# Optimization experiments

Hardware: AMD Instinct MI355X
Metric: run time of the kernel (lower is better)

Reference implementation:

```python
import jax, jax.numpy as jnp
import numpy as np

N_NODES = 100000
N_EDGES = 1600000
IN_C = 128
HID_C = 128   # 2 * out_channels
OUT_C = 64


def gcn_conv(x, row, col, w, W, b, num_nodes):
    """PyG GCNConv: linear transform, add self-loops (weight 1),
    symmetric degree normalization, scatter-sum aggregation, bias."""
    h = x @ W  # [N, C_out]
    loop = jnp.arange(num_nodes, dtype=row.dtype)
    r = jnp.concatenate([row, loop])
    c = jnp.concatenate([col, loop])
    ew = jnp.concatenate([w, jnp.ones((num_nodes,), dtype=w.dtype)])
    deg = jax.ops.segment_sum(ew, c, num_segments=num_nodes)
    dinv = jnp.where(deg > 0, jax.lax.rsqrt(deg), 0.0)
    norm = dinv[r] * ew * dinv[c]            # [E+N]
    msg = h[r] * norm[:, None]               # [E+N, C_out] gather
    out = jax.ops.segment_sum(msg, c, num_segments=num_nodes)
    return out + b


def setup_inputs() -> dict:
    key = jax.random.key(0)
    k1, k2, k3, k4, k5, k6, k7, k8 = jax.random.split(key, 8)
    x = jax.random.normal(k1, (N_NODES, IN_C), dtype=jnp.float32)
    edge_index = jax.random.randint(k2, (2, N_EDGES), 0, N_NODES, dtype=jnp.int64)
    edge_weight = jax.random.uniform(k3, (N_EDGES,), dtype=jnp.float32)
    s1 = float(np.sqrt(6.0 / (IN_C + HID_C)))
    s2 = float(np.sqrt(6.0 / (HID_C + OUT_C)))
    W1 = jax.random.uniform(k4, (IN_C, HID_C), minval=-s1, maxval=s1, dtype=jnp.float32)
    b1 = jnp.zeros((HID_C,), dtype=jnp.float32)
    W2 = jax.random.uniform(k5, (HID_C, OUT_C), minval=-s2, maxval=s2, dtype=jnp.float32)
    b2 = jnp.zeros((OUT_C,), dtype=jnp.float32)
    return {"x": x, "edge_index": edge_index, "edge_weight": edge_weight,
            "W1": W1, "b1": b1, "W2": W2, "b2": b2}


def reference(x, edge_index, edge_weight, W1, b1, W2, b2):
    row, col = edge_index[0], edge_index[1]
    n = x.shape[0]
    h = jax.nn.relu(gcn_conv(x, row, col, edge_weight, W1, b1, n))
    h = jax.nn.relu(gcn_conv(h, row, col, edge_weight, W2, b2, n))
    return h
```

## Files before the change

### kernel.cpp

```cpp
#include <hip/hip_runtime.h>

#define TPB 256

typedef unsigned int uint32;
typedef unsigned short ushort_t;
typedef __attribute__((ext_vector_type(8))) short bf16x8;
typedef __attribute__((ext_vector_type(4))) float f32x4;

constexpr int NB = 256;
constexpr int B1 = 256;

__device__ __forceinline__ uint32 pack_bf16x2(float a, float b) {
  uint32 ua = __float_as_uint(a), ub = __float_as_uint(b);
  ua += 0x7FFFu + ((ua >> 16) & 1u);
  ub += 0x7FFFu + ((ub >> 16) & 1u);
  return (ua >> 16) | (ub & 0xFFFF0000u);
}
__device__ __forceinline__ ushort_t bf16_of(float a) {
  uint32 u = __float_as_uint(a);
  u += 0x7FFFu + ((u >> 16) & 1u);
  return (ushort_t)(u >> 16);
}
__device__ __forceinline__ float bf16_lo(uint32 u) { return __uint_as_float(u << 16); }
__device__ __forceinline__ float bf16_hi(uint32 u) { return __uint_as_float(u & 0xFFFF0000u); }

__global__ __launch_bounds__(256) void rx_hist(const int* __restrict__ col,
                                               int* __restrict__ blockhist, int e, int chunk) {
  __shared__ int h[NB];
  int tid = threadIdx.x, blk = blockIdx.x;
  h[tid] = 0;
  __syncthreads();
  int s = blk * chunk, t = min(e, s + chunk);
  for (int i = s + tid; i < t; i += 256) atomicAdd(&h[col[i] & 255], 1);
  __syncthreads();
  blockhist[tid * B1 + blk] = h[tid];
}

__global__ __launch_bounds__(256) void k_scan1(int* __restrict__ a, int* __restrict__ bsum, int n) {
  __shared__ int s[256];
  int tid = threadIdx.x;
  int base = blockIdx.x * 1024 + tid * 4;
  int v0 = 0, v1 = 0, v2 = 0, v3 = 0;
  if (base + 0 < n) v0 = a[base + 0];
  if (base + 1 < n) v1 = a[base + 1];
  if (base + 2 < n) v2 = a[base + 2];
  if (base + 3 < n) v3 = a[base + 3];
  int tsum = v0 + v1 + v2 + v3;
  s[tid] = tsum;
  __syncthreads();
  for (int off = 1; off < 256; off <<= 1) {
    int t = (tid >= off) ? s[tid - off] : 0;
    __syncthreads();
    s[tid] += t;
    __syncthreads();
  }
  if (tid == 255) bsum[blockIdx.x] = s[255];
  int e0 = s[tid] - tsum;
  int e1 = e0 + v0, e2 = e1 + v1, e3 = e2 + v2;
  if (base + 0 < n) a[base + 0] = e0;
  if (base + 1 < n) a[base + 1] = e1;
  if (base + 2 < n) a[base + 2] = e2;
  if (base + 3 < n) a[base + 3] = e3;
}

__global__ __launch_bounds__(256) void k_scan2(int* __restrict__ bsum, int nb) {
  __shared__ int s[256];
  int tid = threadIdx.x;
  int v = (tid < nb) ? bsum[tid] : 0;
  s[tid] = v;
  __syncthreads();
  for (int off = 1; off < 256; off <<= 1) {
    int t = (tid >= off) ? s[tid - off] : 0;
    __syncthreads();
    s[tid] += t;
    __syncthreads();
  }
  if (tid < nb) bsum[tid] = s[tid] - v;
}

__global__ void k_scan3b(int* __restrict__ a, const int* __restrict__ bsum, int n) {
  int i = blockIdx.x * TPB + threadIdx.x;
  if (i < n) a[i] += bsum[i >> 10];
}

__global__ __launch_bounds__(256) void rx_scatter1(const int* __restrict__ row,
                                                   const int* __restrict__ col,
                                                   const float* __restrict__ w,
                                                   const int* __restrict__ scanned,
                                                   int4* __restrict__ rec, int e, int chunk) {
  __shared__ int cur[NB];
  int tid = threadIdx.x, blk = blockIdx.x;
  cur[tid] = scanned[tid * B1 + blk];
  __syncthreads();
  int s = blk * chunk, t = min(e, s + chunk);
  for (int i = s + tid; i < t; i += 256) {
    int c = col[i];
    int p = atomicAdd(&cur[c & 255], 1);
    rec[p] = make_int4(row[i], c, __float_as_int(w[i]), 0);
  }
}

__global__ __launch_bounds__(256) void rx_build(const int4* __restrict__ rec,
                                                const int* __restrict__ scanned,
                                                int2* __restrict__ nodeRange,
                                                float* __restrict__ dinv,
                                                int2* __restrict__ edges, int n, int e) {
  constexpr int NH = 512;
  __shared__ int cnt[NH];
  __shared__ int pref[NH];
  __shared__ int cur[NH];
  __shared__ float dw[NH];
  __shared__ int ssum[256];
  int tid = threadIdx.x, lo = blockIdx.x;
  int s = scanned[lo * B1];
  int t = (lo == NB - 1) ? e : scanned[(lo + 1) * B1];
  cnt[tid] = 0; cnt[tid + 256] = 0;
  dw[tid] = 0.f; dw[tid + 256] = 0.f;
  __syncthreads();
  for (int i = s + tid; i < t; i += 256) {
    int4 r = rec[i];
    int hi = ((uint32)r.y) >> 8;
    atomicAdd(&cnt[hi], 1);
    atomicAdd(&dw[hi], __int_as_float(r.z));
  }
  __syncthreads();
  int a0 = cnt[2 * tid], a1 = cnt[2 * tid + 1];
  int sum2 = a0 + a1;
  ssum[tid] = sum2;
  __syncthreads();
  for (int off = 1; off < 256; off <<= 1) {
    int v = (tid >= off) ? ssum[tid - off] : 0;
    __syncthreads();
    ssum[tid] += v;
    __syncthreads();
  }
  int excl = ssum[tid] - sum2;
  pref[2 * tid] = excl;
  pref[2 * tid + 1] = excl + a0;
  __syncthreads();
#pragma unroll
  for (int k = 0; k < 2; ++k) {
    int hi = tid + k * 256;
    int node = (hi << 8) | lo;
    cur[hi] = s + pref[hi];
    if (node < n) {
      nodeRange[node] = make_int2(s + pref[hi], cnt[hi]);
      dinv[node] = rsqrtf(1.0f + dw[hi]);
    }
  }
  __syncthreads();
  for (int i = s + tid; i < t; i += 256) {
    int4 r = rec[i];
    int hi = ((uint32)r.y) >> 8;
    int p = atomicAdd(&cur[hi], 1);
    edges[p] = make_int2(r.x, r.z);
  }
}

__global__ void k_wprep(const float* __restrict__ W, ushort_t* __restrict__ Wt, int K, int M) {
  int i = blockIdx.x * TPB + threadIdx.x;
  if (i < K * M) {
    int k = i / M, m = i % M;
    Wt[m * K + k] = bf16_of(W[i]);
  }
}

template <int M, bool XF32>
__global__ __launch_bounds__(256) void k_gemm_mfma(
    const void* __restrict__ Xv, const ushort_t* __restrict__ Wt,
    const float* __restrict__ dinv, uint32* __restrict__ Hb, int n) {
  __shared__ __align__(16) char smem[16384 + M * 256];
  char* Xs = smem;
  char* Ws = smem + 16384;
  const int tid = threadIdx.x;
  const int lane = tid & 63;
  const int w = tid >> 6;
  const int row0 = blockIdx.x * 64;

  {
    const uint4* src = (const uint4*)Wt;
    for (int idx = tid; idx < M * 16; idx += 256) {
      int r = idx >> 4, g = idx & 15;
      uint4 v = src[idx];
      *(uint4*)(Ws + ((r << 8) | ((g << 4) ^ ((r & 7) << 4)))) = v;
    }
  }
  if constexpr (XF32) {
    const float4* src = (const float4*)Xv;
    for (int idx = tid; idx < 64 * 16; idx += 256) {
      int r = idx >> 4, g = idx & 15;
      int grow = row0 + r;
      float4 va = make_float4(0.f, 0.f, 0.f, 0.f), vb = va;
      if (grow < n) {
        va = src[(size_t)grow * 32 + g * 2];
        vb = src[(size_t)grow * 32 + g * 2 + 1];
      }
      uint4 p;
      p.x = pack_bf16x2(va.x, va.y);
      p.y = pack_bf16x2(va.z, va.w);
      p.z = pack_bf16x2(vb.x, vb.y);
      p.w = pack_bf16x2(vb.z, vb.w);
      *(uint4*)(Xs + ((r << 8) | ((g << 4) ^ ((r & 7) << 4)))) = p;
    }
  } else {
    const uint4* src = (const uint4*)Xv;
    for (int idx = tid; idx < 64 * 16; idx += 256) {
      int r = idx >> 4, g = idx & 15;
      int grow = row0 + r;
      uint4 v = make_uint4(0u, 0u, 0u, 0u);
      if (grow < n) v = src[(size_t)grow * 16 + g];
      *(uint4*)(Xs + ((r << 8) | ((g << 4) ^ ((r & 7) << 4)))) = v;
    }
  }
  __syncthreads();

  constexpr int CT = M / 16;
  f32x4 acc[CT];
#pragma unroll
  for (int c = 0; c < CT; ++c) acc[c] = (f32x4){0.f, 0.f, 0.f, 0.f};

  const int arow = (w << 4) | (lane & 15);
  const int kb0 = (lane >> 4) << 4;
#pragma unroll
  for (int ks = 0; ks < 4; ++ks) {
    int kbyte = ks * 64 + kb0;
    bf16x8 a = *(const bf16x8*)(Xs + ((arow << 8) | (kbyte ^ ((arow & 7) << 4))));
#pragma unroll
    for (int c = 0; c < CT; ++c) {
      int brow = c * 16 + (lane & 15);
      bf16x8 b = *(const bf16x8*)(Ws + ((brow << 8) | (kbyte ^ ((brow & 7) << 4))));
      acc[c] = __builtin_amdgcn_mfma_f32_16x16x32_bf16(a, b, acc[c], 0, 0, 0);
    }
  }
  __syncthreads();

  ushort_t* Cs = (ushort_t*)smem;
  const int rbase = (w << 4) | ((lane >> 4) << 2);
  float dv[4];
#pragma unroll
  for (int r = 0; r < 4; ++r) {
    int g = row0 + rbase + r;
    dv[r] = (g < n) ? dinv[g] : 0.f;
  }
#pragma unroll
  for (int c = 0; c < CT; ++c) {
    int col = c * 16 + (lane & 15);
#pragma unroll
    for (int r = 0; r < 4; ++r)
      Cs[(rbase + r) * 132 + col] = bf16_of(acc[c][r] * dv[r]);
  }
  __syncthreads();
  constexpr int G2 = M / 4;
  uint2* dst = (uint2*)Hb;
  for (int idx = tid; idx < 64 * G2; idx += 256) {
    int r = idx / G2, g = idx % G2;
    int grow = row0 + r;
    if (grow < n)
      dst[(size_t)grow * G2 + g] = *(const uint2*)((const char*)Cs + r * 264 + g * 8);
  }
}

template <int C>
__global__ __launch_bounds__(TPB) void k_agg(
    const uint32* __restrict__ hsb, const int2* __restrict__ edges,
    const int2* __restrict__ nodeRange, const float* __restrict__ dinv,
    const float* __restrict__ bias, void* __restrict__ out, int n) {
  int gwave = (blockIdx.x * TPB + threadIdx.x) >> 6;
  int lane = threadIdx.x & 63;
  int half = lane >> 5;
  int hl = lane & 31;
  int node = gwave * 2 + half;
  if (node >= n) return;
  int2 nr = nodeRange[node];
  int s0 = nr.x, s1 = nr.x + nr.y;
  float di = dinv[node];

  if constexpr (C == 128) {
    const uint2* h2 = (const uint2*)hsb;
    uint2 u = h2[(size_t)node * 32 + hl];
    float a0 = bf16_lo(u.x), a1 = bf16_hi(u.x);
    float a2 = bf16_lo(u.y), a3 = bf16_hi(u.y);
    int k = s0;
    for (; k + 3 < s1; k += 4) {
      int2 e0 = edges[k], e1 = edges[k + 1], e2 = edges[k + 2], e3 = edges[k + 3];
      uint2 v0 = h2[(size_t)e0.x * 32 + hl];
      uint2 v1 = h2[(size_t)e1.x * 32 + hl];
      uint2 v2 = h2[(size_t)e2.x * 32 + hl];
      uint2 v3 = h2[(size_t)e3.x * 32 + hl];
      float w0 = __int_as_float(e0.y), w1 = __int_as_float(e1.y);
      float w2 = __int_as_float(e2.y), w3 = __int_as_float(e3.y);
      a0 = fmaf(bf16_lo(v0.x), w0, a0); a1 = fmaf(bf16_hi(v0.x), w0, a1);
      a2 = fmaf(bf16_lo(v0.y), w0, a2); a3 = fmaf(bf16_hi(v0.y), w0, a3);
      a0 = fmaf(bf16_lo(v1.x), w1, a0); a1 = fmaf(bf16_hi(v1.x), w1, a1);
      a2 = fmaf(bf16_lo(v1.y), w1, a2); a3 = fmaf(bf16_hi(v1.y), w1, a3);
      a0 = fmaf(bf16_lo(v2.x), w2, a0); a1 = fmaf(bf16_hi(v2.x), w2, a1);
      a2 = fmaf(bf16_lo(v2.y), w2, a2); a3 = fmaf(bf16_hi(v2.y), w2, a3);
      a0 = fmaf(bf16_lo(v3.x), w3, a0); a1 = fmaf(bf16_hi(v3.x), w3, a1);
      a2 = fmaf(bf16_lo(v3.y), w3, a2); a3 = fmaf(bf16_hi(v3.y), w3, a3);
    }
    for (; k < s1; ++k) {
      int2 ee = edges[k];
      uint2 v = h2[(size_t)ee.x * 32 + hl];
      float wv = __int_as_float(ee.y);
      a0 = fmaf(bf16_lo(v.x), wv, a0); a1 = fmaf(bf16_hi(v.x), wv, a1);
      a2 = fmaf(bf16_lo(v.y), wv, a2); a3 = fmaf(bf16_hi(v.y), wv, a3);
    }
    float4 bb = ((const float4*)bias)[hl];
    uint2 ob;
    ob.x = pack_bf16x2(fmaxf(fmaf(a0, di, bb.x), 0.f), fmaxf(fmaf(a1, di, bb.y), 0.f));
    ob.y = pack_bf16x2(fmaxf(fmaf(a2, di, bb.z), 0.f), fmaxf(fmaf(a3, di, bb.w), 0.f));
    ((uint2*)out)[(size_t)node * 32 + hl] = ob;
  } else {
    const uint32* h = hsb;
    uint32 u = h[(size_t)node * 32 + hl];
    float a0 = bf16_lo(u), a1 = bf16_hi(u);
    int k = s0;
    for (; k + 3 < s1; k += 4) {
      int2 e0 = edges[k], e1 = edges[k + 1], e2 = edges[k + 2], e3 = edges[k + 3];
      uint32 v0 = h[(size_t)e0.x * 32 + hl];
      uint32 v1 = h[(size_t)e1.x * 32 + hl];
      uint32 v2 = h[(size_t)e2.x * 32 + hl];
      uint32 v3 = h[(size_t)e3.x * 32 + hl];
      float w0 = __int_as_float(e0.y), w1 = __int_as_float(e1.y);
      float w2 = __int_as_float(e2.y), w3 = __int_as_float(e3.y);
      a0 = fmaf(bf16_lo(v0), w0, a0); a1 = fmaf(bf16_hi(v0), w0, a1);
      a0 = fmaf(bf16_lo(v1), w1, a0); a1 = fmaf(bf16_hi(v1), w1, a1);
      a0 = fmaf(bf16_lo(v2), w2, a0); a1 = fmaf(bf16_hi(v2), w2, a1);
      a0 = fmaf(bf16_lo(v3), w3, a0); a1 = fmaf(bf16_hi(v3), w3, a1);
    }
    for (; k < s1; ++k) {
      int2 ee = edges[k];
      uint32 v = h[(size_t)ee.x * 32 + hl];
      float wv = __int_as_float(ee.y);
      a0 = fmaf(bf16_lo(v), wv, a0); a1 = fmaf(bf16_hi(v), wv, a1);
    }
    float2 bb = ((const float2*)bias)[hl];
    float2 o;
    o.x = fmaxf(fmaf(a0, di, bb.x), 0.f);
    o.y = fmaxf(fmaf(a1, di, bb.y), 0.f);
    ((float2*)out)[(size_t)node * 32 + hl] = o;
  }
}

extern "C" void kernel_launch(void* const* d_in, const int* in_sizes, int n_in,
                              void* d_out, int out_size, void* d_ws, size_t ws_size,
                              hipStream_t stream) {
  const float* x  = (const float*)d_in[0];
  const int*   ei = (const int*)d_in[1];
  const float* ew = (const float*)d_in[2];
  const float* W1 = (const float*)d_in[3];
  const float* b1 = (const float*)d_in[4];
  const float* W2 = (const float*)d_in[5];
  const float* b2 = (const float*)d_in[6];
  float* out = (float*)d_out;

  constexpr int IN_C = 128, HID = 128, OUTC = 64;
  const int n = in_sizes[0] / IN_C;
  const int e = in_sizes[2];
  const int* rowp = ei;
  const int* colp = ei + e;

  auto cdiv = [](long a, long b) { return (int)((a + b - 1) / b); };
  auto align = [](size_t v) { return (v + 255) & ~(size_t)255; };

  char* ws = (char*)d_ws;
  size_t o = 0;
  int*      blockhist = (int*)(ws + o);     o = align(o + (size_t)NB * B1 * 4);
  int*      bsum      = (int*)(ws + o);     o = align(o + 4096);
  float*    dinv      = (float*)(ws + o);   o = align(o + (size_t)n * 4);
  int2*     nodeRange = (int2*)(ws + o);    o = align(o + (size_t)n * 8);
  ushort_t* Wt1       = (ushort_t*)(ws + o); o = align(o + (size_t)HID * IN_C * 2);
  ushort_t* Wt2       = (ushort_t*)(ws + o); o = align(o + (size_t)OUTC * HID * 2);
  int4*     rec       = (int4*)(ws + o);    o = align(o + (size_t)e * 16);
  int2*     edges     = (int2*)(ws + o);    o = align(o + (size_t)e * 8);
  uint32*   hs1b      = (uint32*)(ws + o);  o = align(o + (size_t)n * (HID / 2) * 4);
  uint32*   o1b       = (uint32*)(ws + o);  o = align(o + (size_t)n * (HID / 2) * 4);
  uint32*   hs2b      = hs1b;

  const int chunk = cdiv(e, B1);
  const int nscan = NB * B1;

  rx_hist<<<B1, 256, 0, stream>>>(colp, blockhist, e, chunk);
  k_wprep<<<cdiv(IN_C * HID, TPB), TPB, 0, stream>>>(W1, Wt1, IN_C, HID);
  k_wprep<<<cdiv(HID * OUTC, TPB), TPB, 0, stream>>>(W2, Wt2, HID, OUTC);
  k_scan1<<<nscan / 1024, 256, 0, stream>>>(blockhist, bsum, nscan);
  k_scan2<<<1, 256, 0, stream>>>(bsum, nscan / 1024);
  k_scan3b<<<nscan / TPB, TPB, 0, stream>>>(blockhist, bsum, nscan);
  rx_scatter1<<<B1, 256, 0, stream>>>(rowp, colp, ew, blockhist, rec, e, chunk);
  rx_build<<<NB, 256, 0, stream>>>(rec, blockhist, nodeRange, dinv, edges, n, e);

  k_gemm_mfma<HID, true><<<cdiv(n, 64), 256, 0, stream>>>(x, Wt1, dinv, hs1b, n);
  k_agg<HID><<<cdiv((long)n * 32, TPB), TPB, 0, stream>>>(hs1b, edges, nodeRange, dinv, b1, o1b, n);

  k_gemm_mfma<OUTC, false><<<cdiv(n, 64), 256, 0, stream>>>(o1b, Wt2, dinv, hs2b, n);
  k_agg<OUTC><<<cdiv((long)n * 32, TPB), TPB, 0, stream>>>(hs2b, edges, nodeRange, dinv, b2, out, n);
}
```

Baseline: 210.3 us.

## Use one wave per node with 4-way edge split in aggregation; pack sort records

The aggregation kernels now give each node a full 64-lane wave. Four 16-lane groups each walk every fourth edge, use wider 16-byte (layer 1) or 8-byte (layer 2) row loads, and are combined with cross-lane shuffle reductions. The radix-sort intermediate record shrinks from 16 to 8 bytes by packing the column's high bits into the row field, which halves that traffic. The two weight-prep launches are merged into one. Risks: the shuffle reduction adds overhead, lanes sit idle on low-degree nodes, and the packing assumes row indices fit in 20 bits.

```diff
diff --git a/kernel.cpp b/kernel.cpp
--- a/kernel.cpp
+++ b/kernel.cpp
@@ -87,7 +87,7 @@
                                                    const int* __restrict__ col,
                                                    const float* __restrict__ w,
                                                    const int* __restrict__ scanned,
-                                                   int4* __restrict__ rec, int e, int chunk) {
+                                                   int2* __restrict__ rec, int e, int chunk) {
   __shared__ int cur[NB];
   int tid = threadIdx.x, blk = blockIdx.x;
   cur[tid] = scanned[tid * B1 + blk];
@@ -96,11 +96,11 @@
   for (int i = s + tid; i < t; i += 256) {
     int c = col[i];
     int p = atomicAdd(&cur[c & 255], 1);
-    rec[p] = make_int4(row[i], c, __float_as_int(w[i]), 0);
-  }
-}
-
-__global__ __launch_bounds__(256) void rx_build(const int4* __restrict__ rec,
+    rec[p] = make_int2(row[i] | ((c >> 8) << 20), __float_as_int(w[i]));
+  }
+}
+
+__global__ __launch_bounds__(256) void rx_build(const int2* __restrict__ rec,
                                                 const int* __restrict__ scanned,
                                                 int2* __restrict__ nodeRange,
                                                 float* __restrict__ dinv,
@@ -118,10 +118,10 @@
   dw[tid] = 0.f; dw[tid + 256] = 0.f;
   __syncthreads();
   for (int i = s + tid; i < t; i += 256) {
-    int4 r = rec[i];
-    int hi = ((uint32)r.y) >> 8;
+    int2 r = rec[i];
+    int hi = ((uint32)r.x) >> 20;
     atomicAdd(&cnt[hi], 1);
-    atomicAdd(&dw[hi], __int_as_float(r.z));
+    atomicAdd(&dw[hi], __int_as_float(r.y));
   }
   __syncthreads();
   int a0 = cnt[2 * tid], a1 = cnt[2 * tid + 1];
@@ -150,18 +150,25 @@
   }
   __syncthreads();
   for (int i = s + tid; i < t; i += 256) {
-    int4 r = rec[i];
-    int hi = ((uint32)r.y) >> 8;
+    int2 r = rec[i];
+    int hi = ((uint32)r.x) >> 20;
     int p = atomicAdd(&cur[hi], 1);
-    edges[p] = make_int2(r.x, r.z);
-  }
-}
-
-__global__ void k_wprep(const float* __restrict__ W, ushort_t* __restrict__ Wt, int K, int M) {
+    edges[p] = make_int2(r.x & 0xFFFFF, r.y);
+  }
+}
+
+__global__ void k_wprep2(const float* __restrict__ W1, ushort_t* __restrict__ Wt1,
+                         const float* __restrict__ W2, ushort_t* __restrict__ Wt2) {
   int i = blockIdx.x * TPB + threadIdx.x;
-  if (i < K * M) {
-    int k = i / M, m = i % M;
-    Wt[m * K + k] = bf16_of(W[i]);
+  if (i < 128 * 128) {
+    int k = i >> 7, m = i & 127;
+    Wt1[m * 128 + k] = bf16_of(W1[i]);
+  } else {
+    int j = i - 128 * 128;
+    if (j < 128 * 64) {
+      int k = j >> 6, m = j & 63;
+      Wt2[m * 128 + k] = bf16_of(W2[j]);
+    }
   }
 }
 
@@ -265,80 +272,107 @@
     const uint32* __restrict__ hsb, const int2* __restrict__ edges,
     const int2* __restrict__ nodeRange, const float* __restrict__ dinv,
     const float* __restrict__ bias, void* __restrict__ out, int n) {
-  int gwave = (blockIdx.x * TPB + threadIdx.x) >> 6;
+  int node = (blockIdx.x * TPB + threadIdx.x) >> 6;
+  if (node >= n) return;
   int lane = threadIdx.x & 63;
-  int half = lane >> 5;
-  int hl = lane & 31;
-  int node = gwave * 2 + half;
-  if (node >= n) return;
+  int g = lane >> 4;
+  int gl = lane & 15;
   int2 nr = nodeRange[node];
   int s0 = nr.x, s1 = nr.x + nr.y;
   float di = dinv[node];
 
   if constexpr (C == 128) {
+    const uint4* h4 = (const uint4*)hsb;
+    float a0, a1, a2, a3, a4, a5, a6, a7;
+    if (g == 0) {
+      uint4 u = h4[(size_t)node * 16 + gl];
+      a0 = bf16_lo(u.x); a1 = bf16_hi(u.x); a2 = bf16_lo(u.y); a3 = bf16_hi(u.y);
+      a4 = bf16_lo(u.z); a5 = bf16_hi(u.z); a6 = bf16_lo(u.w); a7 = bf16_hi(u.w);
+    } else {
+      a0 = a1 = a2 = a3 = a4 = a5 = a6 = a7 = 0.f;
+    }
+    int k = s0 + g;
+    for (; k + 4 < s1; k += 8) {
+      int2 e0 = edges[k], e1 = edges[k + 4];
+      uint4 v0 = h4[(size_t)e0.x * 16 + gl];
+      uint4 v1 = h4[(size_t)e1.x * 16 + gl];
+      float w0 = __int_as_float(e0.y), w1 = __int_as_float(e1.y);
+      a0 = fmaf(bf16_lo(v0.x), w0, a0); a1 = fmaf(bf16_hi(v0.x), w0, a1);
+      a2 = fmaf(bf16_lo(v0.y), w0, a2); a3 = fmaf(bf16_hi(v0.y), w0, a3);
+      a4 = fmaf(bf16_lo(v0.z), w0, a4); a5 = fmaf(bf16_hi(v0.z), w0, a5);
+      a6 = fmaf(bf16_lo(v0.w), w0, a6); a7 = fmaf(bf16_hi(v0.w), w0, a7);
+      a0 = fmaf(bf16_lo(v1.x), w1, a0); a1 = fmaf(bf16_hi(v1.x), w1, a1);
+      a2 = fmaf(bf16_lo(v1.y), w1, a2); a3 = fmaf(bf16_hi(v1.y), w1, a3);
+      a4 = fmaf(bf16_lo(v1.z), w1, a4); a5 = fmaf(bf16_hi(v1.z), w1, a5);
+      a6 = fmaf(bf16_lo(v1.w), w1, a6); a7 = fmaf(bf16_hi(v1.w), w1, a7);
+    }
+    if (k < s1) {
+      int2 e0 = edges[k];
+      uint4 v0 = h4[(size_t)e0.x * 16 + gl];
+      float w0 = __int_as_float(e0.y);
+      a0 = fmaf(bf16_lo(v0.x), w0, a0); a1 = fmaf(bf16_hi(v0.x), w0, a1);
+      a2 = fmaf(bf16_lo(v0.y), w0, a2); a3 = fmaf(bf16_hi(v0.y), w0, a3);
+      a4 = fmaf(bf16_lo(v0.z), w0, a4); a5 = fmaf(bf16_hi(v0.z), w0, a5);
+      a6 = fmaf(bf16_lo(v0.w), w0, a6); a7 = fmaf(bf16_hi(v0.w), w0, a7);
+    }
+    a0 += __shfl_xor(a0, 16); a1 += __shfl_xor(a1, 16);
+    a2 += __shfl_xor(a2, 16); a3 += __shfl_xor(a3, 16);
+    a4 += __shfl_xor(a4, 16); a5 += __shfl_xor(a5, 16);
+    a6 += __shfl_xor(a6, 16); a7 += __shfl_xor(a7, 16);
+    a0 += __shfl_xor(a0, 32); a1 += __shfl_xor(a1, 32);
+    a2 += __shfl_xor(a2, 32); a3 += __shfl_xor(a3, 32);
+    a4 += __shfl_xor(a4, 32); a5 += __shfl_xor(a5, 32);
+    a6 += __shfl_xor(a6, 32); a7 += __shfl_xor(a7, 32);
+    if (g == 0) {
+      float4 bb0 = ((const float4*)bias)[gl * 2];
+      float4 bb1 = ((const float4*)bias)[gl * 2 + 1];
+      uint4 ob;
+      ob.x = pack_bf16x2(fmaxf(fmaf(a0, di, bb0.x), 0.f), fmaxf(fmaf(a1, di, bb0.y), 0.f));
+      ob.y = pack_bf16x2(fmaxf(fmaf(a2, di, bb0.z), 0.f), fmaxf(fmaf(a3, di, bb0.w), 0.f));
+      ob.z = pack_bf16x2(fmaxf(fmaf(a4, di, bb1.x), 0.f), fmaxf(fmaf(a5, di, bb1.y), 0.f));
+      ob.w = pack_bf16x2(fmaxf(fmaf(a6, di, bb1.z), 0.f), fmaxf(fmaf(a7, di, bb1.w), 0.f));
+      ((uint4*)out)[(size_t)node * 16 + gl] = ob;
+    }
+  } else {
     const uint2* h2 = (const uint2*)hsb;
-    uint2 u = h2[(size_t)node * 32 + hl];
-    float a0 = bf16_lo(u.x), a1 = bf16_hi(u.x);
-    float a2 = bf16_lo(u.y), a3 = bf16_hi(u.y);
-    int k = s0;
-    for (; k + 3 < s1; k += 4) {
-      int2 e0 = edges[k], e1 = edges[k + 1], e2 = edges[k + 2], e3 = edges[k + 3];
-      uint2 v0 = h2[(size_t)e0.x * 32 + hl];
-      uint2 v1 = h2[(size_t)e1.x * 32 + hl];
-      uint2 v2 = h2[(size_t)e2.x * 32 + hl];
-      uint2 v3 = h2[(size_t)e3.x * 32 + hl];
+    float a0, a1, a2, a3;
+    if (g == 0) {
+      uint2 u = h2[(size_t)node * 16 + gl];
+      a0 = bf16_lo(u.x); a1 = bf16_hi(u.x); a2 = bf16_lo(u.y); a3 = bf16_hi(u.y);
+    } else {
+      a0 = a1 = a2 = a3 = 0.f;
+    }
+    int k = s0 + g;
+    for (; k + 4 < s1; k += 8) {
+      int2 e0 = edges[k], e1 = edges[k + 4];
+      uint2 v0 = h2[(size_t)e0.x * 16 + gl];
+      uint2 v1 = h2[(size_t)e1.x * 16 + gl];
       float w0 = __int_as_float(e0.y), w1 = __int_as_float(e1.y);
-      float w2 = __int_as_float(e2.y), w3 = __int_as_float(e3.y);
       a0 = fmaf(bf16_lo(v0.x), w0, a0); a1 = fmaf(bf16_hi(v0.x), w0, a1);
       a2 = fmaf(bf16_lo(v0.y), w0, a2); a3 = fmaf(bf16_hi(v0.y), w0, a3);
       a0 = fmaf(bf16_lo(v1.x), w1, a0); a1 = fmaf(bf16_hi(v1.x), w1, a1);
       a2 = fmaf(bf16_lo(v1.y), w1, a2); a3 = fmaf(bf16_hi(v1.y), w1, a3);
-      a0 = fmaf(bf16_lo(v2.x), w2, a0); a1 = fmaf(bf16_hi(v2.x), w2, a1);
-      a2 = fmaf(bf16_lo(v2.y), w2, a2); a3 = fmaf(bf16_hi(v2.y), w2, a3);
-      a0 = fmaf(bf16_lo(v3.x), w3, a0); a1 = fmaf(bf16_hi(v3.x), w3, a1);
-      a2 = fmaf(bf16_lo(v3.y), w3, a2); a3 = fmaf(bf16_hi(v3.y), w3, a3);
-    }
-    for (; k < s1; ++k) {
-      int2 ee = edges[k];
-      uint2 v = h2[(size_t)ee.x * 32 + hl];
-      float wv = __int_as_float(ee.y);
-      a0 = fmaf(bf16_lo(v.x), wv, a0); a1 = fmaf(bf16_hi(v.x), wv, a1);
-      a2 = fmaf(bf16_lo(v.y), wv, a2); a3 = fmaf(bf16_hi(v.y), wv, a3);
-    }
-    float4 bb = ((const float4*)bias)[hl];
-    uint2 ob;
-    ob.x = pack_bf16x2(fmaxf(fmaf(a0, di, bb.x), 0.f), fmaxf(fmaf(a1, di, bb.y), 0.f));
-    ob.y = pack_bf16x2(fmaxf(fmaf(a2, di, bb.z), 0.f), fmaxf(fmaf(a3, di, bb.w), 0.f));
-    ((uint2*)out)[(size_t)node * 32 + hl] = ob;
-  } else {
-    const uint32* h = hsb;
-    uint32 u = h[(size_t)node * 32 + hl];
-    float a0 = bf16_lo(u), a1 = bf16_hi(u);
-    int k = s0;
-    for (; k + 3 < s1; k += 4) {
-      int2 e0 = edges[k], e1 = edges[k + 1], e2 = edges[k + 2], e3 = edges[k + 3];
-      uint32 v0 = h[(size_t)e0.x * 32 + hl];
-      uint32 v1 = h[(size_t)e1.x * 32 + hl];
-      uint32 v2 = h[(size_t)e2.x * 32 + hl];
-      uint32 v3 = h[(size_t)e3.x * 32 + hl];
-      float w0 = __int_as_float(e0.y), w1 = __int_as_float(e1.y);
-      float w2 = __int_as_float(e2.y), w3 = __int_as_float(e3.y);
-      a0 = fmaf(bf16_lo(v0), w0, a0); a1 = fmaf(bf16_hi(v0), w0, a1);
-      a0 = fmaf(bf16_lo(v1), w1, a0); a1 = fmaf(bf16_hi(v1), w1, a1);
-      a0 = fmaf(bf16_lo(v2), w2, a0); a1 = fmaf(bf16_hi(v2), w2, a1);
-      a0 = fmaf(bf16_lo(v3), w3, a0); a1 = fmaf(bf16_hi(v3), w3, a1);
-    }
-    for (; k < s1; ++k) {
-      int2 ee = edges[k];
-      uint32 v = h[(size_t)ee.x * 32 + hl];
-      float wv = __int_as_float(ee.y);
-      a0 = fmaf(bf16_lo(v), wv, a0); a1 = fmaf(bf16_hi(v), wv, a1);
-    }
-    float2 bb = ((const float2*)bias)[hl];
-    float2 o;
-    o.x = fmaxf(fmaf(a0, di, bb.x), 0.f);
-    o.y = fmaxf(fmaf(a1, di, bb.y), 0.f);
-    ((float2*)out)[(size_t)node * 32 + hl] = o;
+    }
+    if (k < s1) {
+      int2 e0 = edges[k];
+      uint2 v0 = h2[(size_t)e0.x * 16 + gl];
+      float w0 = __int_as_float(e0.y);
+      a0 = fmaf(bf16_lo(v0.x), w0, a0); a1 = fmaf(bf16_hi(v0.x), w0, a1);
+      a2 = fmaf(bf16_lo(v0.y), w0, a2); a3 = fmaf(bf16_hi(v0.y), w0, a3);
+    }
+    a0 += __shfl_xor(a0, 16); a1 += __shfl_xor(a1, 16);
+    a2 += __shfl_xor(a2, 16); a3 += __shfl_xor(a3, 16);
+    a0 += __shfl_xor(a0, 32); a1 += __shfl_xor(a1, 32);
+    a2 += __shfl_xor(a2, 32); a3 += __shfl_xor(a3, 32);
+    if (g == 0) {
+      float4 bb = ((const float4*)bias)[gl];
+      float4 o;
+      o.x = fmaxf(fmaf(a0, di, bb.x), 0.f);
+      o.y = fmaxf(fmaf(a1, di, bb.y), 0.f);
+      o.z = fmaxf(fmaf(a2, di, bb.z), 0.f);
+      o.w = fmaxf(fmaf(a3, di, bb.w), 0.f);
+      ((float4*)out)[(size_t)node * 16 + gl] = o;
+    }
   }
 }
 
@@ -371,7 +405,7 @@
   int2*     nodeRange = (int2*)(ws + o);    o = align(o + (size_t)n * 8);
   ushort_t* Wt1       = (ushort_t*)(ws + o); o = align(o + (size_t)HID * IN_C * 2);
   ushort_t* Wt2       = (ushort_t*)(ws + o); o = align(o + (size_t)OUTC * HID * 2);
-  int4*     rec       = (int4*)(ws + o);    o = align(o + (size_t)e * 16);
+  int2*     rec       = (int2*)(ws + o);    o = align(o + (size_t)e * 8);
   int2*     edges     = (int2*)(ws + o);    o = align(o + (size_t)e * 8);
   uint32*   hs1b      = (uint32*)(ws + o);  o = align(o + (size_t)n * (HID / 2) * 4);
   uint32*   o1b       = (uint32*)(ws + o);  o = align(o + (size_t)n * (HID / 2) * 4);
@@ -381,8 +415,7 @@
   const int nscan = NB * B1;
 
   rx_hist<<<B1, 256, 0, stream>>>(colp, blockhist, e, chunk);
-  k_wprep<<<cdiv(IN_C * HID, TPB), TPB, 0, stream>>>(W1, Wt1, IN_C, HID);
-  k_wprep<<<cdiv(HID * OUTC, TPB), TPB, 0, stream>>>(W2, Wt2, HID, OUTC);
+  k_wprep2<<<cdiv(IN_C * HID + HID * OUTC, TPB), TPB, 0, stream>>>(W1, Wt1, W2, Wt2);
   k_scan1<<<nscan / 1024, 256, 0, stream>>>(blockhist, bsum, nscan);
   k_scan2<<<1, 256, 0, stream>>>(bsum, nscan / 1024);
   k_scan3b<<<nscan / TPB, TPB, 0, stream>>>(blockhist, bsum, nscan);
@@ -390,8 +423,8 @@
   rx_build<<<NB, 256, 0, stream>>>(rec, blockhist, nodeRange, dinv, edges, n, e);
 
   k_gemm_mfma<HID, true><<<cdiv(n, 64), 256, 0, stream>>>(x, Wt1, dinv, hs1b, n);
-  k_agg<HID><<<cdiv((long)n * 32, TPB), TPB, 0, stream>>>(hs1b, edges, nodeRange, dinv, b1, o1b, n);
+  k_agg<HID><<<cdiv(n, 4), TPB, 0, stream>>>(hs1b, edges, nodeRange, dinv, b1, o1b, n);
 
   k_gemm_mfma<OUTC, false><<<cdiv(n, 64), 256, 0, stream>>>(o1b, Wt2, dinv, hs2b, n);
-  k_agg<OUTC><<<cdiv((long)n * 32, TPB), TPB, 0, stream>>>(hs2b, edges, nodeRange, dinv, b2, out, n);
-}
+  k_agg<OUTC><<<cdiv(n, 4), TPB, 0, stream>>>(hs2b, edges, nodeRange, dinv, b2, out, n);
+}
```

Measured after the change: 210.2 us. About the same (-0.0%).
